# Kernel optimization log

Hardware: AMD Instinct MI355X
Metric: run time of the kernel (lower is better)

Reference implementation:

```python
import jax, jax.numpy as jnp
import numpy as np

# Qwen3-Next-like dims
B, S, HID = 2, 2048, 2048
H, KV, D, ROT = 16, 2, 128, 32
G = H // KV              # kv repeat groups
SCALE = D ** -0.5
EPS = 1e-6
BETA_BIAS, BIAS_CAP = 1.0, 3.0   # L1 logit bias
BETA_POST = 0.5                  # L2 post-softmax rescale
ALPHA_K, ALPHA_V = 0.1, 0.1      # L4 k/v rescale
GMIN, GMAX = 0.9, 1.1
EMIN, EMAX = 0.9, 1.1


def setup_inputs() -> dict:
    key = jax.random.key(0)
    ks = jax.random.split(key, 10)
    hidden_states = jax.random.normal(ks[0], (B, S, HID), jnp.float32)
    # partial rotary embeddings (rot_dim = head_dim // 4)
    pos = jnp.arange(S, dtype=jnp.float32)
    inv = 1.0 / (10000.0 ** (jnp.arange(0, ROT, 2, dtype=jnp.float32) / ROT))
    freqs = pos[:, None] * inv[None, :]
    emb = jnp.concatenate([freqs, freqs], axis=-1)          # [S, ROT]
    cos = jnp.broadcast_to(jnp.cos(emb)[None], (B, S, ROT)).astype(jnp.float32)
    sin = jnp.broadcast_to(jnp.sin(emb)[None], (B, S, ROT)).astype(jnp.float32)
    # additive causal mask [B,1,S,S]
    causal = jnp.tril(jnp.ones((S, S), jnp.bool_))
    attention_mask = jnp.where(causal, 0.0, -1e9).astype(jnp.float32)
    attention_mask = jnp.broadcast_to(attention_mask[None, None], (B, 1, S, S))
    # key prior: positive, sums to 1 over kv_len
    prior = jax.nn.softmax(jax.random.normal(ks[1], (S,), jnp.float32))
    s = 0.02
    Wq = jax.random.normal(ks[2], (HID, H * D * 2), jnp.float32) * s
    Wk = jax.random.normal(ks[3], (HID, KV * D), jnp.float32) * s
    Wv = jax.random.normal(ks[4], (HID, KV * D), jnp.float32) * s
    Wo = jax.random.normal(ks[5], (H * D, HID), jnp.float32) * s
    q_norm_w = 1.0 + 0.02 * jax.random.normal(ks[6], (D,), jnp.float32)
    k_norm_w = 1.0 + 0.02 * jax.random.normal(ks[7], (D,), jnp.float32)
    return {"hidden_states": hidden_states, "cos": cos, "sin": sin,
            "attention_mask": attention_mask, "prior": prior,
            "Wq": Wq, "Wk": Wk, "Wv": Wv, "Wo": Wo,
            "q_norm_w": q_norm_w, "k_norm_w": k_norm_w}


def _rms(x, w):
    return x * jax.lax.rsqrt(jnp.mean(x * x, axis=-1, keepdims=True) + EPS) * w


def _rot_half(x):
    x1, x2 = jnp.split(x, 2, axis=-1)
    return jnp.concatenate([-x2, x1], axis=-1)


def _rope(x, cos, sin):
    # x: [B,h,S,D]; rotary on first ROT dims only (Qwen3-Next partial rotary)
    xr, xp = x[..., :ROT], x[..., ROT:]
    xr = xr * cos + _rot_half(xr) * sin
    return jnp.concatenate([xr, xp], axis=-1)


def reference(hidden_states, cos, sin, attention_mask, prior, Wq, Wk, Wv, Wo, q_norm_w, k_norm_w):
    h = hidden_states
    # gated q projection: chunk into query + gate
    qg = (h @ Wq).reshape(B, S, H, 2 * D)
    q, gate = qg[..., :D], qg[..., D:]
    gate = gate.reshape(B, S, H * D)
    q = _rms(q, q_norm_w).transpose(0, 2, 1, 3)                       # [B,H,S,D]
    k = _rms((h @ Wk).reshape(B, S, KV, D), k_norm_w).transpose(0, 2, 1, 3)  # [B,KV,S,D]
    v = (h @ Wv).reshape(B, S, KV, D).transpose(0, 2, 1, 3)
    c, s_ = cos[:, None], sin[:, None]                                # [B,1,S,ROT]
    q, k = _rope(q, c, s_), _rope(k, c, s_)
    k = jnp.repeat(k, G, axis=1)                                      # GQA expand -> [B,H,S,D]
    v = jnp.repeat(v, G, axis=1)
    # L4: prior-based elementwise k/v rescale with clamped gamma/eta
    pc = prior * S                                                    # mean ~1 over keys
    gamma = jnp.clip(1.0 + ALPHA_K * (pc - 1.0), GMIN, GMAX)
    eta = jnp.clip(1.0 + ALPHA_V * (pc - 1.0), EMIN, EMAX)
    k = k * gamma[None, None, :, None]
    v = v * eta[None, None, :, None]
    scores = jnp.einsum('bhqd,bhkd->bhqk', q, k) * SCALE
    # L1: capped steering bias on logits
    scores = scores + jnp.clip(BETA_BIAS * prior, -BIAS_CAP, BIAS_CAP)[None, None, None, :]
    scores = scores + attention_mask
    probs = jax.nn.softmax(scores.astype(jnp.float32), axis=-1)       # fp32 softmax
    # L2: post-softmax prior rescale + renorm
    p2 = probs * (1.0 + BETA_POST * pc)[None, None, None, :]
    probs = p2 / jnp.sum(p2, axis=-1, keepdims=True)
    out = jnp.einsum('bhqk,bhkd->bhqd', probs.astype(h.dtype), v)
    out = out.transpose(0, 2, 1, 3).reshape(B, S, H * D)
    out = out * jax.nn.sigmoid(gate)                                  # gated attention output
    return out @ Wo
```

## Files before the change

### kernel.cpp

```cpp
#include <hip/hip_runtime.h>
#include <hip/hip_bf16.h>
#include <stdint.h>

#define B_    2
#define S_    2048
#define HID_  2048
#define H_    16
#define KV_   2
#define D_    128
#define ROT_  32
#define NQG   4096
#define SCALE_ 0.08838834764831845f

typedef __attribute__((ext_vector_type(8))) short  short8;
typedef __attribute__((ext_vector_type(4))) float  floatx4;

__device__ __forceinline__ float b2f(unsigned short u) {
  union { unsigned int i; float f; } v; v.i = ((unsigned int)u) << 16; return v.f;
}
__device__ __forceinline__ unsigned short f2b(float f) {
  union { float f; unsigned int i; } v; v.f = f;
  return (unsigned short)((v.i + 0x7fffu + ((v.i >> 16) & 1u)) >> 16);
}
__device__ __forceinline__ void gload_lds16(const unsigned short* g, unsigned short* l) {
  __builtin_amdgcn_global_load_lds((const __attribute__((address_space(1))) void*)g,
                                   (__attribute__((address_space(3))) void*)l, 16, 0, 0);
}

__device__ __forceinline__ void transpose_body(const float* __restrict__ in,
                                               unsigned short* __restrict__ out,
                                               int R, int C, int bx, int by, int t) {
  __shared__ unsigned short tile[64][68];
  int tx = t & 15, ty = t >> 4;
  long c0 = (long)bx * 64, r0 = (long)by * 64;
#pragma unroll
  for (int i = 0; i < 4; i++) {
    int row = ty + 16 * i;
    const float* src = in + (r0 + row) * C + c0 + 4 * tx;
    float4 v = *(const float4*)src;
    tile[row][4 * tx + 0] = f2b(v.x);
    tile[row][4 * tx + 1] = f2b(v.y);
    tile[row][4 * tx + 2] = f2b(v.z);
    tile[row][4 * tx + 3] = f2b(v.w);
  }
  __syncthreads();
#pragma unroll
  for (int i = 0; i < 4; i++) {
    int oc = ty + 16 * i;
    ushort4 v;
    v.x = tile[4 * tx + 0][oc];
    v.y = tile[4 * tx + 1][oc];
    v.z = tile[4 * tx + 2][oc];
    v.w = tile[4 * tx + 3][oc];
    *(ushort4*)(out + (c0 + oc) * R + r0 + 4 * tx) = v;
  }
}

__global__ __launch_bounds__(256) void k_preproc(const float* __restrict__ h_f,
                                                 const float* __restrict__ prior,
                                                 const float* __restrict__ Wq,
                                                 const float* __restrict__ Wk,
                                                 const float* __restrict__ Wv,
                                                 const float* __restrict__ Wo,
                                                 unsigned short* __restrict__ hb,
                                                 unsigned short* __restrict__ WqT,
                                                 unsigned short* __restrict__ WkvT,
                                                 unsigned short* __restrict__ WoT,
                                                 float* __restrict__ ge,
                                                 float* __restrict__ kbias) {
  int bx = blockIdx.x;
  const int t = threadIdx.x;
  if (bx < 8) {
    int i = bx * 256 + t;
    float p  = prior[i];
    float pc = p * (float)S_;
    float g  = 1.0f + 0.1f * (pc - 1.0f);
    g = fminf(fmaxf(g, 0.9f), 1.1f);
    ge[i] = g;
    float cb = fminf(fmaxf(p, -3.0f), 3.0f);
    kbias[i] = cb + logf(1.0f + 0.5f * pc);
    return;
  }
  bx -= 8;
  if (bx < 4096) {
    long i0 = ((long)bx * 256 + t) * 8;
    float4 a = *(const float4*)(h_f + i0);
    float4 b = *(const float4*)(h_f + i0 + 4);
    short8 v;
    v[0] = (short)f2b(a.x); v[1] = (short)f2b(a.y);
    v[2] = (short)f2b(a.z); v[3] = (short)f2b(a.w);
    v[4] = (short)f2b(b.x); v[5] = (short)f2b(b.y);
    v[6] = (short)f2b(b.z); v[7] = (short)f2b(b.w);
    *(short8*)(hb + i0) = v;
    return;
  }
  bx -= 4096;
  if (bx < 2048) { transpose_body(Wq, WqT, 2048, 4096, bx & 63, bx >> 6, t); return; }
  bx -= 2048;
  if (bx < 1024) { transpose_body(Wo, WoT, 2048, 2048, bx & 31, bx >> 5, t); return; }
  bx -= 1024;
  if (bx < 128)  { transpose_body(Wk, WkvT, 2048, 256, bx & 3, bx >> 2, t); return; }
  bx -= 128;
  transpose_body(Wv, WkvT + (size_t)256 * 2048, 2048, 256, bx & 3, bx >> 2, t);
}

template <int OUT32>
__global__ __launch_bounds__(256) void k_gemm_bt(const unsigned short* __restrict__ A,
                                                 const unsigned short* __restrict__ Bt,
                                                 void* __restrict__ Cv,
                                                 int M, int N, int K) {
  __shared__ __align__(16) unsigned short As[2][128 * 32];
  __shared__ __align__(16) unsigned short Bs[2][128 * 32];
  const int t    = threadIdx.x;
  const int lane = t & 63;
  const int wv   = t >> 6;
  const int wm   = wv >> 1, wn = wv & 1;
  const long m0  = (long)blockIdx.y * 128;
  const long n0  = (long)blockIdx.x * 128;
  const int r15  = lane & 15, g4 = lane >> 4;

  const int srow = lane >> 2;
  const int scol = ((lane & 3) ^ ((lane >> 2) & 3)) * 8;
  const unsigned short* sA0 = A  + (m0 + wv * 16 + srow)       * K + scol;
  const unsigned short* sA1 = A  + (m0 + (wv + 4) * 16 + srow) * K + scol;
  const unsigned short* sB0 = Bt + (n0 + wv * 16 + srow)       * K + scol;
  const unsigned short* sB1 = Bt + (n0 + (wv + 4) * 16 + srow) * K + scol;

  floatx4 acc[4][4];
#pragma unroll
  for (int m = 0; m < 4; m++)
#pragma unroll
    for (int n = 0; n < 4; n++) acc[m][n] = (floatx4){0.f, 0.f, 0.f, 0.f};

  gload_lds16(sA0, &As[0][wv * 512]);
  gload_lds16(sA1, &As[0][(wv + 4) * 512]);
  gload_lds16(sB0, &Bs[0][wv * 512]);
  gload_lds16(sB1, &Bs[0][(wv + 4) * 512]);
  __syncthreads();

  const int fcol = (g4 ^ (r15 & 3)) * 8;
  int cur = 0;
  for (int k0 = 0; k0 < K; k0 += 32) {
    if (k0 + 32 < K) {
      const int nx = cur ^ 1, ko = k0 + 32;
      gload_lds16(sA0 + ko, &As[nx][wv * 512]);
      gload_lds16(sA1 + ko, &As[nx][(wv + 4) * 512]);
      gload_lds16(sB0 + ko, &Bs[nx][wv * 512]);
      gload_lds16(sB1 + ko, &Bs[nx][(wv + 4) * 512]);
    }
    short8 af[4], bf[4];
#pragma unroll
    for (int m = 0; m < 4; m++)
      af[m] = *(const short8*)(&As[cur][(wm * 64 + m * 16 + r15) * 32 + fcol]);
#pragma unroll
    for (int n = 0; n < 4; n++)
      bf[n] = *(const short8*)(&Bs[cur][(wn * 64 + n * 16 + r15) * 32 + fcol]);
#pragma unroll
    for (int m = 0; m < 4; m++)
#pragma unroll
      for (int n = 0; n < 4; n++)
        acc[m][n] = __builtin_amdgcn_mfma_f32_16x16x32_bf16(af[m], bf[n], acc[m][n], 0, 0, 0);
    __syncthreads();
    cur ^= 1;
  }

#pragma unroll
  for (int m = 0; m < 4; m++) {
    const long rbase = m0 + wm * 64 + m * 16 + g4 * 4;
#pragma unroll
    for (int n = 0; n < 4; n++) {
      const long cidx = n0 + wn * 64 + n * 16 + r15;
#pragma unroll
      for (int i = 0; i < 4; i++) {
        if (OUT32) ((float*)Cv)[(rbase + i) * N + cidx] = acc[m][n][i];
        else ((unsigned short*)Cv)[(rbase + i) * N + cidx] = f2b(acc[m][n][i]);
      }
    }
  }
}

__global__ __launch_bounds__(256) void k_qkvpost(const unsigned short* __restrict__ qg,
                                                 const unsigned short* __restrict__ kvraw,
                                                 const float* __restrict__ cosb,
                                                 const float* __restrict__ sinb,
                                                 const float* __restrict__ ge,
                                                 const float* __restrict__ qnw,
                                                 const float* __restrict__ knw,
                                                 unsigned short* __restrict__ qT,
                                                 unsigned short* __restrict__ kF,
                                                 unsigned short* __restrict__ vF) {
  int bxx = blockIdx.x;
  if (bxx < 18432) {
    int wid  = (bxx * 256 + (int)threadIdx.x) >> 6;
    int lane = threadIdx.x & 63;
    int r    = wid % (H_ + KV_);
    long bs  = wid / (H_ + KV_);
    int b = (int)(bs >> 11), s = (int)(bs & 2047);
    int d0 = lane * 2;

    float x0, x1;
    if (r < H_) {
      const unsigned short* src = qg + bs * NQG + r * 256 + d0;
      x0 = b2f(src[0]); x1 = b2f(src[1]);
    } else {
      const unsigned short* src = kvraw + bs * 512 + (r - H_) * 128 + d0;
      x0 = b2f(src[0]); x1 = b2f(src[1]);
    }
    float ss = x0 * x0 + x1 * x1;
#pragma unroll
    for (int mask = 1; mask < 64; mask <<= 1) ss += __shfl_xor(ss, mask);
    float rstd = rsqrtf(ss * (1.0f / 128.0f) + 1e-6f);
    float w0, w1;
    if (r < H_) { w0 = qnw[d0]; w1 = qnw[d0 + 1]; }
    else        { w0 = knw[d0]; w1 = knw[d0 + 1]; }
    float xn0 = x0 * rstd * w0, xn1 = x1 * rstd * w1;
    float p0 = __shfl_xor(xn0, 8), p1 = __shfl_xor(xn1, 8);
    float y0 = xn0, y1 = xn1;
    if (lane < 16) {
      float c0 = cosb[bs * ROT_ + d0], c1 = cosb[bs * ROT_ + d0 + 1];
      float s0 = sinb[bs * ROT_ + d0], s1 = sinb[bs * ROT_ + d0 + 1];
      float sgn = (lane < 8) ? -1.0f : 1.0f;
      y0 = xn0 * c0 + sgn * p0 * s0;
      y1 = xn1 * c1 + sgn * p1 * s1;
    }
    if (r < H_) {
      unsigned int pack = (unsigned int)f2b(y0) | ((unsigned int)f2b(y1) << 16);
      *(unsigned int*)(qT + ((long)(b * H_ + r) * S_ + s) * D_ + d0) = pack;
    } else {
      float g = ge[s];
      unsigned int pack = (unsigned int)f2b(y0 * g) | ((unsigned int)f2b(y1 * g) << 16);
      int kvb = r - H_;
      size_t off = (size_t)(b * KV_ + kvb) * 262144
                 + (size_t)((s >> 4) * 4 + (d0 >> 5)) * 512
                 + (size_t)(((s & 15) + (((d0 >> 3) & 3)) * 16)) * 8 + (d0 & 7);
      *(unsigned int*)(kF + off) = pack;
    }
  } else {
    int bx  = bxx - 18432;
    int scn = bx & 7, d = (bx >> 3) & 127, kvb = (bx >> 10) & 1, b = bx >> 11;
    int s = scn * 256 + threadIdx.x;
    float v = b2f(kvraw[((long)(b * S_ + s)) * 512 + 256 + kvb * 128 + d]);
    v *= ge[s];
    size_t off = (size_t)(b * KV_ + kvb) * 262144
               + (size_t)((s >> 6) * 16 + (d >> 4) * 2 + ((s >> 5) & 1)) * 512
               + (size_t)((d & 15) + ((s >> 3) & 3) * 16) * 8 + (s & 7);
    vF[off] = f2b(v);
  }
}

__global__ __launch_bounds__(256) void k_attn(const unsigned short* __restrict__ qT,
                                              const unsigned short* __restrict__ kF,
                                              const unsigned short* __restrict__ vF,
                                              const float* __restrict__ kbias,
                                              const unsigned short* __restrict__ qg,
                                              unsigned short* __restrict__ ag) {
  __shared__ __align__(16) unsigned short KL[2][8192];
  __shared__ __align__(16) unsigned short Ps[4][16 * 88];
  const int t = threadIdx.x;
  const int lane = t & 63, wv = t >> 6;
  const int r15 = lane & 15, g4 = lane >> 4;
  const int p = blockIdx.x;
  const int xcd = p & 7;
  const int grp = xcd >> 1;
  const int mem = ((p >> 3) << 1) | (xcd & 1);
  const int head = mem & 7;
  const int quad = 31 - (mem >> 3);
  const int b = grp >> 1, kvh = grp & 1;
  const int hh = kvh * 8 + head;
  const int strip = quad * 4 + wv;
  const int q0s = strip * 16;
  const int ntiles = quad + 1;

  const unsigned short* kFg = kF + (size_t)(b * KV_ + kvh) * 262144;
  const unsigned short* vFg = vF + (size_t)(b * KV_ + kvh) * 262144;

  short8 qf[4];
  {
    const unsigned short* qp = qT + ((long)(b * H_ + hh) * S_ + q0s + r15) * D_ + g4 * 8;
#pragma unroll
    for (int kb = 0; kb < 4; kb++) qf[kb] = *(const short8*)(qp + kb * 32);
  }

  floatx4 oacc[8];
#pragma unroll
  for (int nd = 0; nd < 8; nd++) oacc[nd] = (floatx4){0.f, 0.f, 0.f, 0.f};
  float mrow = -1e30f, lrw = 0.f;

#pragma unroll
  for (int i = 0; i < 4; i++)
    gload_lds16(kFg + (size_t)wv * 2048 + i * 512 + lane * 8, &KL[0][wv * 2048 + i * 512]);
  __syncthreads();

  int cur = 0;
  for (int tile = 0; tile < ntiles; tile++) {
    if (tile + 1 < ntiles) {
      const size_t src = (size_t)(tile + 1) * 8192 + wv * 2048 + lane * 8;
#pragma unroll
      for (int i = 0; i < 4; i++)
        gload_lds16(kFg + src + i * 512, &KL[cur ^ 1][wv * 2048 + i * 512]);
    }

    floatx4 sacc[4];
#pragma unroll
    for (int n = 0; n < 4; n++) sacc[n] = (floatx4){0.f, 0.f, 0.f, 0.f};
#pragma unroll
    for (int n = 0; n < 4; n++) {
      const unsigned short* kl = &KL[cur][n * 2048 + lane * 8];
      short8 a0 = *(const short8*)(kl);
      short8 a1 = *(const short8*)(kl + 512);
      short8 a2 = *(const short8*)(kl + 1024);
      short8 a3 = *(const short8*)(kl + 1536);
      sacc[n] = __builtin_amdgcn_mfma_f32_16x16x32_bf16(a0, qf[0], sacc[n], 0, 0, 0);
      sacc[n] = __builtin_amdgcn_mfma_f32_16x16x32_bf16(a1, qf[1], sacc[n], 0, 0, 0);
      sacc[n] = __builtin_amdgcn_mfma_f32_16x16x32_bf16(a2, qf[2], sacc[n], 0, 0, 0);
      sacc[n] = __builtin_amdgcn_mfma_f32_16x16x32_bf16(a3, qf[3], sacc[n], 0, 0, 0);
    }

    const unsigned short* vt = vFg + (size_t)tile * 8192 + lane * 8;
    short8 vfA[8];
#pragma unroll
    for (int nd = 0; nd < 8; nd++) vfA[nd] = *(const short8*)(vt + (nd * 2) * 512);

    const bool last = (tile == ntiles - 1);
    float scf[4][4];
#pragma unroll
    for (int n = 0; n < 4; n++) {
      const int j0 = tile * 64;
      float4 kb4 = *(const float4*)(&kbias[j0 + n * 16 + g4 * 4]);
#pragma unroll
      for (int i = 0; i < 4; i++) {
        float kbv = (i == 0) ? kb4.x : (i == 1) ? kb4.y : (i == 2) ? kb4.z : kb4.w;
        float v = sacc[n][i] * SCALE_ + kbv;
        if (last) {
          int jg = j0 + n * 16 + g4 * 4 + i;
          if (jg > q0s + r15) v = -1e30f;
        }
        scf[n][i] = v;
      }
    }
    float pmax = scf[0][0];
#pragma unroll
    for (int n = 0; n < 4; n++)
#pragma unroll
      for (int i = 0; i < 4; i++) pmax = fmaxf(pmax, scf[n][i]);
    pmax = fmaxf(pmax, __shfl_xor(pmax, 16));
    pmax = fmaxf(pmax, __shfl_xor(pmax, 32));
    if (__any(pmax > mrow + 8.0f)) {
      float mn = fmaxf(mrow, pmax);
      float aq = __expf(mrow - mn);
      mrow = mn;
      lrw *= aq;
      float ai[4];
#pragma unroll
      for (int i = 0; i < 4; i++) ai[i] = __shfl(aq, g4 * 4 + i);
#pragma unroll
      for (int nd = 0; nd < 8; nd++)
#pragma unroll
        for (int i = 0; i < 4; i++) oacc[nd][i] *= ai[i];
    }
    float rsum = 0.f;
#pragma unroll
    for (int n = 0; n < 4; n++)
#pragma unroll
      for (int i = 0; i < 4; i++) {
        float pv = __expf(scf[n][i] - mrow);
        scf[n][i] = pv;
        rsum += pv;
      }
    rsum += __shfl_xor(rsum, 16);
    rsum += __shfl_xor(rsum, 32);
    lrw += rsum;

#pragma unroll
    for (int n = 0; n < 4; n++) {
      unsigned int lo = (unsigned int)f2b(scf[n][0]) | ((unsigned int)f2b(scf[n][1]) << 16);
      unsigned int hi = (unsigned int)f2b(scf[n][2]) | ((unsigned int)f2b(scf[n][3]) << 16);
      uint2 w; w.x = lo; w.y = hi;
      *(uint2*)(&Ps[wv][r15 * 88 + n * 16 + g4 * 4]) = w;
    }

    short8 vfB[8];
#pragma unroll
    for (int nd = 0; nd < 8; nd++) vfB[nd] = *(const short8*)(vt + (nd * 2 + 1) * 512);

    {
      short8 pa0 = *(const short8*)(&Ps[wv][r15 * 88 + g4 * 8]);
#pragma unroll
      for (int nd = 0; nd < 8; nd++)
        oacc[nd] = __builtin_amdgcn_mfma_f32_16x16x32_bf16(pa0, vfA[nd], oacc[nd], 0, 0, 0);
      short8 pa1 = *(const short8*)(&Ps[wv][r15 * 88 + 32 + g4 * 8]);
#pragma unroll
      for (int nd = 0; nd < 8; nd++)
        oacc[nd] = __builtin_amdgcn_mfma_f32_16x16x32_bf16(pa1, vfB[nd], oacc[nd], 0, 0, 0);
    }
    __syncthreads();
    cur ^= 1;
  }

  float il[4];
#pragma unroll
  for (int i = 0; i < 4; i++) il[i] = __shfl(lrw, g4 * 4 + i);
#pragma unroll
  for (int i = 0; i < 4; i++) {
    int q = q0s + g4 * 4 + i;
    float inv = 1.0f / il[i];
    const unsigned short* gptr = qg + ((size_t)(b * S_ + q)) * NQG + hh * 256 + 128;
    unsigned short* aptr = ag + ((size_t)(b * S_ + q)) * (H_ * D_) + hh * D_;
#pragma unroll
    for (int nd = 0; nd < 8; nd++) {
      int d = nd * 16 + r15;
      float gt = b2f(gptr[d]);
      float sg = 1.0f / (1.0f + __expf(-gt));
      aptr[d] = f2b(oacc[nd][i] * inv * sg);
    }
  }
}

extern "C" void kernel_launch(void* const* d_in, const int* in_sizes, int n_in,
                              void* d_out, int out_size, void* d_ws, size_t ws_size,
                              hipStream_t stream) {
  const float* h_f   = (const float*)d_in[0];
  const float* cosb  = (const float*)d_in[1];
  const float* sinb  = (const float*)d_in[2];
  const float* prior = (const float*)d_in[4];
  const float* Wq    = (const float*)d_in[5];
  const float* Wk    = (const float*)d_in[6];
  const float* Wv    = (const float*)d_in[7];
  const float* Wo    = (const float*)d_in[8];
  const float* qnw   = (const float*)d_in[9];
  const float* knw   = (const float*)d_in[10];

  char* ws = (char*)d_ws;
  size_t off = 0;
  auto alloc = [&](size_t bytes) { char* p = ws + off; off += (bytes + 255) & ~(size_t)255; return p; };
  unsigned short* hb    = (unsigned short*)alloc((size_t)4096 * 2048 * 2);
  unsigned short* WqT   = (unsigned short*)alloc((size_t)4096 * 2048 * 2);
  unsigned short* WkvT  = (unsigned short*)alloc((size_t)512 * 2048 * 2);
  unsigned short* WoT   = (unsigned short*)alloc((size_t)2048 * 2048 * 2);
  unsigned short* qg    = (unsigned short*)alloc((size_t)4096 * 4096 * 2);
  unsigned short* kvraw = (unsigned short*)alloc((size_t)4096 * 512 * 2);
  unsigned short* qTb   = (unsigned short*)alloc((size_t)B_ * H_ * S_ * D_ * 2);
  unsigned short* kF    = (unsigned short*)alloc((size_t)B_ * KV_ * S_ * D_ * 2);
  unsigned short* vF    = (unsigned short*)alloc((size_t)B_ * KV_ * S_ * D_ * 2);
  float* ge    = (float*)alloc((size_t)S_ * 4);
  float* kbias = (float*)alloc((size_t)S_ * 4);
  unsigned short* ag = hb;

  dim3 blk(256);
  k_preproc<<<dim3(7432), blk, 0, stream>>>(h_f, prior, Wq, Wk, Wv, Wo,
                                            hb, WqT, WkvT, WoT, ge, kbias);
  k_gemm_bt<0><<<dim3(32, 32), blk, 0, stream>>>(hb, WqT, qg, 4096, 4096, 2048);
  k_gemm_bt<0><<<dim3(4, 32),  blk, 0, stream>>>(hb, WkvT, kvraw, 4096, 512, 2048);
  k_qkvpost<<<dim3(22528), blk, 0, stream>>>(qg, kvraw, cosb, sinb, ge, qnw, knw, qTb, kF, vF);
  k_attn<<<dim3(1024), blk, 0, stream>>>(qTb, kF, vF, kbias, qg, ag);
  k_gemm_bt<1><<<dim3(16, 32), blk, 0, stream>>>(ag, WoT, d_out, 4096, 2048, 2048);
}
```

Measured before the change: 294.6 us.

## Fuse Q and KV projections into one GEMM, retune LDS swizzle, add MFMA priority

Concatenates the transposed Wq, Wk and Wv weights into a single WqkvT buffer so the Q/gate and K/V projections run as one GEMM with N=4608. This removes a separate small, under-occupied launch, and downstream kernels now read from the combined qgkv buffer with a new row stride. The LDS XOR swizzle in the GEMM changes to key off different row bits, aiming to reduce bank conflicts. s_setprio hints are also placed around the MFMA blocks in attention. The risk is that the swizzle change must stay consistent between the store and load sides; both are changed together here.

```diff
diff --git a/kernel.cpp b/kernel.cpp
--- a/kernel.cpp
+++ b/kernel.cpp
@@ -9,7 +9,7 @@
 #define KV_   2
 #define D_    128
 #define ROT_  32
-#define NQG   4096
+#define QGS   4608
 #define SCALE_ 0.08838834764831845f
 
 typedef __attribute__((ext_vector_type(8))) short  short8;
@@ -63,8 +63,7 @@
                                                  const float* __restrict__ Wv,
                                                  const float* __restrict__ Wo,
                                                  unsigned short* __restrict__ hb,
-                                                 unsigned short* __restrict__ WqT,
-                                                 unsigned short* __restrict__ WkvT,
+                                                 unsigned short* __restrict__ WqkvT,
                                                  unsigned short* __restrict__ WoT,
                                                  float* __restrict__ ge,
                                                  float* __restrict__ kbias) {
@@ -95,13 +94,13 @@
     return;
   }
   bx -= 4096;
-  if (bx < 2048) { transpose_body(Wq, WqT, 2048, 4096, bx & 63, bx >> 6, t); return; }
+  if (bx < 2048) { transpose_body(Wq, WqkvT, 2048, 4096, bx & 63, bx >> 6, t); return; }
   bx -= 2048;
   if (bx < 1024) { transpose_body(Wo, WoT, 2048, 2048, bx & 31, bx >> 5, t); return; }
   bx -= 1024;
-  if (bx < 128)  { transpose_body(Wk, WkvT, 2048, 256, bx & 3, bx >> 2, t); return; }
+  if (bx < 128)  { transpose_body(Wk, WqkvT + (size_t)4096 * 2048, 2048, 256, bx & 3, bx >> 2, t); return; }
   bx -= 128;
-  transpose_body(Wv, WkvT + (size_t)256 * 2048, 2048, 256, bx & 3, bx >> 2, t);
+  transpose_body(Wv, WqkvT + (size_t)4352 * 2048, 2048, 256, bx & 3, bx >> 2, t);
 }
 
 template <int OUT32>
@@ -120,7 +119,7 @@
   const int r15  = lane & 15, g4 = lane >> 4;
 
   const int srow = lane >> 2;
-  const int scol = ((lane & 3) ^ ((lane >> 2) & 3)) * 8;
+  const int scol = ((lane & 3) ^ ((lane >> 3) & 3)) * 8;
   const unsigned short* sA0 = A  + (m0 + wv * 16 + srow)       * K + scol;
   const unsigned short* sA1 = A  + (m0 + (wv + 4) * 16 + srow) * K + scol;
   const unsigned short* sB0 = Bt + (n0 + wv * 16 + srow)       * K + scol;
@@ -138,7 +137,7 @@
   gload_lds16(sB1, &Bs[0][(wv + 4) * 512]);
   __syncthreads();
 
-  const int fcol = (g4 ^ (r15 & 3)) * 8;
+  const int fcol = (g4 ^ ((r15 >> 1) & 3)) * 8;
   int cur = 0;
   for (int k0 = 0; k0 < K; k0 += 32) {
     if (k0 + 32 < K) {
@@ -179,8 +178,7 @@
   }
 }
 
-__global__ __launch_bounds__(256) void k_qkvpost(const unsigned short* __restrict__ qg,
-                                                 const unsigned short* __restrict__ kvraw,
+__global__ __launch_bounds__(256) void k_qkvpost(const unsigned short* __restrict__ qgkv,
                                                  const float* __restrict__ cosb,
                                                  const float* __restrict__ sinb,
                                                  const float* __restrict__ ge,
@@ -200,10 +198,10 @@
 
     float x0, x1;
     if (r < H_) {
-      const unsigned short* src = qg + bs * NQG + r * 256 + d0;
+      const unsigned short* src = qgkv + bs * QGS + r * 256 + d0;
       x0 = b2f(src[0]); x1 = b2f(src[1]);
     } else {
-      const unsigned short* src = kvraw + bs * 512 + (r - H_) * 128 + d0;
+      const unsigned short* src = qgkv + bs * QGS + 4096 + (r - H_) * 128 + d0;
       x0 = b2f(src[0]); x1 = b2f(src[1]);
     }
     float ss = x0 * x0 + x1 * x1;
@@ -239,7 +237,7 @@
     int bx  = bxx - 18432;
     int scn = bx & 7, d = (bx >> 3) & 127, kvb = (bx >> 10) & 1, b = bx >> 11;
     int s = scn * 256 + threadIdx.x;
-    float v = b2f(kvraw[((long)(b * S_ + s)) * 512 + 256 + kvb * 128 + d]);
+    float v = b2f(qgkv[((long)(b * S_ + s)) * QGS + 4352 + kvb * 128 + d]);
     v *= ge[s];
     size_t off = (size_t)(b * KV_ + kvb) * 262144
                + (size_t)((s >> 6) * 16 + (d >> 4) * 2 + ((s >> 5) & 1)) * 512
@@ -252,7 +250,7 @@
                                               const unsigned short* __restrict__ kF,
                                               const unsigned short* __restrict__ vF,
                                               const float* __restrict__ kbias,
-                                              const unsigned short* __restrict__ qg,
+                                              const unsigned short* __restrict__ qgkv,
                                               unsigned short* __restrict__ ag) {
   __shared__ __align__(16) unsigned short KL[2][8192];
   __shared__ __align__(16) unsigned short Ps[4][16 * 88];
@@ -303,6 +301,7 @@
     floatx4 sacc[4];
 #pragma unroll
     for (int n = 0; n < 4; n++) sacc[n] = (floatx4){0.f, 0.f, 0.f, 0.f};
+    __builtin_amdgcn_s_setprio(1);
 #pragma unroll
     for (int n = 0; n < 4; n++) {
       const unsigned short* kl = &KL[cur][n * 2048 + lane * 8];
@@ -315,6 +314,7 @@
       sacc[n] = __builtin_amdgcn_mfma_f32_16x16x32_bf16(a2, qf[2], sacc[n], 0, 0, 0);
       sacc[n] = __builtin_amdgcn_mfma_f32_16x16x32_bf16(a3, qf[3], sacc[n], 0, 0, 0);
     }
+    __builtin_amdgcn_s_setprio(0);
 
     const unsigned short* vt = vFg + (size_t)tile * 8192 + lane * 8;
     short8 vfA[8];
@@ -384,6 +384,7 @@
     for (int nd = 0; nd < 8; nd++) vfB[nd] = *(const short8*)(vt + (nd * 2 + 1) * 512);
 
     {
+      __builtin_amdgcn_s_setprio(1);
       short8 pa0 = *(const short8*)(&Ps[wv][r15 * 88 + g4 * 8]);
 #pragma unroll
       for (int nd = 0; nd < 8; nd++)
@@ -392,6 +393,7 @@
 #pragma unroll
       for (int nd = 0; nd < 8; nd++)
         oacc[nd] = __builtin_amdgcn_mfma_f32_16x16x32_bf16(pa1, vfB[nd], oacc[nd], 0, 0, 0);
+      __builtin_amdgcn_s_setprio(0);
     }
     __syncthreads();
     cur ^= 1;
@@ -404,7 +406,7 @@
   for (int i = 0; i < 4; i++) {
     int q = q0s + g4 * 4 + i;
     float inv = 1.0f / il[i];
-    const unsigned short* gptr = qg + ((size_t)(b * S_ + q)) * NQG + hh * 256 + 128;
+    const unsigned short* gptr = qgkv + ((size_t)(b * S_ + q)) * QGS + hh * 256 + 128;
     unsigned short* aptr = ag + ((size_t)(b * S_ + q)) * (H_ * D_) + hh * D_;
 #pragma unroll
     for (int nd = 0; nd < 8; nd++) {
@@ -434,11 +436,9 @@
   size_t off = 0;
   auto alloc = [&](size_t bytes) { char* p = ws + off; off += (bytes + 255) & ~(size_t)255; return p; };
   unsigned short* hb    = (unsigned short*)alloc((size_t)4096 * 2048 * 2);
-  unsigned short* WqT   = (unsigned short*)alloc((size_t)4096 * 2048 * 2);
-  unsigned short* WkvT  = (unsigned short*)alloc((size_t)512 * 2048 * 2);
+  unsigned short* WqkvT = (unsigned short*)alloc((size_t)4608 * 2048 * 2);
   unsigned short* WoT   = (unsigned short*)alloc((size_t)2048 * 2048 * 2);
-  unsigned short* qg    = (unsigned short*)alloc((size_t)4096 * 4096 * 2);
-  unsigned short* kvraw = (unsigned short*)alloc((size_t)4096 * 512 * 2);
+  unsigned short* qgkv  = (unsigned short*)alloc((size_t)4096 * QGS * 2);
   unsigned short* qTb   = (unsigned short*)alloc((size_t)B_ * H_ * S_ * D_ * 2);
   unsigned short* kF    = (unsigned short*)alloc((size_t)B_ * KV_ * S_ * D_ * 2);
   unsigned short* vF    = (unsigned short*)alloc((size_t)B_ * KV_ * S_ * D_ * 2);
@@ -448,10 +448,9 @@
 
   dim3 blk(256);
   k_preproc<<<dim3(7432), blk, 0, stream>>>(h_f, prior, Wq, Wk, Wv, Wo,
-                                            hb, WqT, WkvT, WoT, ge, kbias);
-  k_gemm_bt<0><<<dim3(32, 32), blk, 0, stream>>>(hb, WqT, qg, 4096, 4096, 2048);
-  k_gemm_bt<0><<<dim3(4, 32),  blk, 0, stream>>>(hb, WkvT, kvraw, 4096, 512, 2048);
-  k_qkvpost<<<dim3(22528), blk, 0, stream>>>(qg, kvraw, cosb, sinb, ge, qnw, knw, qTb, kF, vF);
-  k_attn<<<dim3(1024), blk, 0, stream>>>(qTb, kF, vF, kbias, qg, ag);
+                                            hb, WqkvT, WoT, ge, kbias);
+  k_gemm_bt<0><<<dim3(36, 32), blk, 0, stream>>>(hb, WqkvT, qgkv, 4096, QGS, 2048);
+  k_qkvpost<<<dim3(22528), blk, 0, stream>>>(qgkv, cosb, sinb, ge, qnw, knw, qTb, kF, vF);
+  k_attn<<<dim3(1024), blk, 0, stream>>>(qTb, kF, vF, kbias, qgkv, ag);
   k_gemm_bt<1><<<dim3(16, 32), blk, 0, stream>>>(ag, WoT, d_out, 4096, 2048, 2048);
 }
```

Result: faster. 269.4 us (-8.5%).
